# Performance work log

Hardware: AMD Instinct MI355X
Metric: run time of the kernel (lower is better)

The kernel has to match this reference:

```python
import jax, jax.numpy as jnp
import numpy as np


def setup_inputs() -> dict:
    key = jax.random.key(0)
    ks = jax.random.split(key, 5)
    b, c, h, w = 8, 64, 256, 256
    ic = c // 2
    return {
        "x": jax.random.normal(ks[0], (b, c, h, w), dtype=jnp.float32),
        "w_phi": jax.random.normal(ks[1], (ic, c), dtype=jnp.float32) * 0.1,
        "w_theta": jax.random.normal(ks[2], (ic, c), dtype=jnp.float32) * 0.1,
        "w_g": jax.random.normal(ks[3], (ic, c), dtype=jnp.float32) * 0.1,
        "w_mask": jax.random.normal(ks[4], (c, ic), dtype=jnp.float32) * 0.1,
    }


def _conv1x1(x, wgt):
    # bias-free 1x1 conv == channel matmul: (b,c,h,w) x (o,c) -> (b,o,h,w)
    return jnp.einsum('bchw,oc->bohw', x, wgt)


def reference(x, w_phi, w_theta, w_g, w_mask):
    b, c, h, w = x.shape
    ic = c // 2
    n = (h * w) // 2  # per-row length after the quirky view(b, c, -1) of a (b, c/2, h*w) tensor

    # phi and g: conv -> flatten -> global softmax over all c/2*h*w entries -> view (b, c, n)
    phi1 = jax.nn.softmax(_conv1x1(x, w_phi).reshape(b, -1), axis=1).reshape(b, c, n)
    g1 = jax.nn.softmax(_conv1x1(x, w_g).reshape(b, -1), axis=1).reshape(b, c, n)
    theta = _conv1x1(x, w_theta).reshape(b, c, n)

    # y = g1 @ phi1^T @ theta : (b,c,c) then (b,c,n)
    att = jnp.einsum('bcn,bdn->bcd', g1, phi1)
    y = jnp.einsum('bcd,bdn->bcn', att, theta)

    f_s = y.reshape(b, ic, h, w)
    return jnp.einsum('bihw,oi->bohw', f_s, w_mask)
```

## Files before the change

kernel.cpp:

```cpp
#include <hip/hip_runtime.h>

typedef __attribute__((ext_vector_type(8))) short short8;
typedef __attribute__((ext_vector_type(4))) float f32x4;
typedef __attribute__((ext_vector_type(4))) unsigned int uint4v;

#define HW 65536
#define NPOS 32768

__device__ __forceinline__ unsigned short f2bf(float f) {
  unsigned u = __builtin_bit_cast(unsigned, f);
  u += 0x7fffu + ((u >> 16) & 1u);
  return (unsigned short)(u >> 16);
}
__device__ __forceinline__ float bf2f(unsigned short h) {
  unsigned u = (unsigned)h << 16;
  return __builtin_bit_cast(float, u);
}
__device__ __forceinline__ int slot4(int r) { return (r ^ (r >> 2)) & 15; }
__device__ __forceinline__ short8 ld_e16(const unsigned short* p) {
  const uint2 a = *(const uint2*)p;
  const uint2 b = *(const uint2*)(p + 4);
  uint4v u = {a.x, a.y, b.x, b.y};
  return __builtin_bit_cast(short8, u);
}

__global__ __launch_bounds__(256) void k0_prep(
    const float* __restrict__ wphi, const float* __restrict__ wg,
    unsigned short* __restrict__ Whi, unsigned short* __restrict__ Wlo)
{
  const int idx = blockIdx.x * 256 + threadIdx.x;
  const int u = idx >> 6, c = idx & 63;
  const float w = (u < 32) ? wphi[u * 64 + c] : wg[(u - 32) * 64 + c];
  const unsigned short h = f2bf(w);
  Whi[idx] = h;
  Wlo[idx] = f2bf(w - bf2f(h));
}

__global__ __launch_bounds__(256) void k1_att(
    const float* __restrict__ x, const unsigned short* __restrict__ Whi,
    const unsigned short* __restrict__ Wlo, float* __restrict__ attP,
    float2* __restrict__ spart)
{
  __shared__ unsigned short E[2][128 * 68];
  __shared__ float2 rbuf[4];

  const int tid = threadIdx.x;
  const int b = blockIdx.y, blk = blockIdx.x;
  const int w = tid >> 6, l = tid & 63;
  const int lr = l & 15, g = l >> 4;
  const int h = w >> 1, qb = (w & 1) * 2;
  const int n0 = blk * 256;
  const float* xb = x + (size_t)b * 64 * HW + (size_t)h * NPOS;

  short8 wbh[4][2], wbl[4][2];
  #pragma unroll
  for (int cht = 0; cht < 4; ++cht)
    #pragma unroll
    for (int ks = 0; ks < 2; ++ks) {
      const size_t off = (size_t)(cht * 16 + lr) * 64 + ks * 32 + g * 8;
      wbh[cht][ks] = *(const short8*)(Whi + off);
      wbl[cht][ks] = *(const short8*)(Wlo + off);
    }

  f32x4 aacc[4] = {{0.f,0.f,0.f,0.f},{0.f,0.f,0.f,0.f},{0.f,0.f,0.f,0.f},{0.f,0.f,0.f,0.f}};
  float ssp = 0.f, ssg = 0.f;

  float xvA[16], xvB[16];
  #pragma unroll
  for (int e = 0; e < 16; ++e) {
    const size_t co = (size_t)((e >> 3) * 32 + g * 8 + (e & 7)) * HW;
    xvA[e] = xb[co + n0 + (qb + 0) * 16 + lr];
    xvB[e] = xb[co + n0 + (qb + 1) * 16 + lr];
  }

  for (int t = 0; t < 4; ++t) {
    const int buf = t & 1;
    #pragma unroll
    for (int j = 0; j < 2; ++j) {
      const float* xv = j ? xvB : xvA;
      short8 ah[2];
      #pragma unroll
      for (int ks = 0; ks < 2; ++ks)
        #pragma unroll
        for (int e = 0; e < 8; ++e)
          ah[ks][e] = (short)f2bf(xv[ks * 8 + e]);
      f32x4 cacc[4] = {{0.f,0.f,0.f,0.f},{0.f,0.f,0.f,0.f},{0.f,0.f,0.f,0.f},{0.f,0.f,0.f,0.f}};
      #pragma unroll
      for (int cht = 0; cht < 4; ++cht)
        #pragma unroll
        for (int ks = 0; ks < 2; ++ks) {
          cacc[cht] = __builtin_amdgcn_mfma_f32_16x16x32_bf16(ah[ks], wbh[cht][ks], cacc[cht], 0, 0, 0);
          cacc[cht] = __builtin_amdgcn_mfma_f32_16x16x32_bf16(ah[ks], wbl[cht][ks], cacc[cht], 0, 0, 0);
        }
      #pragma unroll
      for (int cht = 0; cht < 4; ++cht) {
        const float e0 = __expf(cacc[cht][0]);
        const float e1 = __expf(cacc[cht][1]);
        const float e2 = __expf(cacc[cht][2]);
        const float e3 = __expf(cacc[cht][3]);
        if (cht < 2) ssp += (e0 + e1) + (e2 + e3);
        else         ssg += (e0 + e1) + (e2 + e3);
        const int row = ((cht >= 2) ? 64 : 0) + 2 * ((cht & 1) * 16 + lr) + h;
        uint2 pk;
        pk.x = (unsigned)f2bf(e0) | ((unsigned)f2bf(e1) << 16);
        pk.y = (unsigned)f2bf(e2) | ((unsigned)f2bf(e3) << 16);
        *(uint2*)&E[buf][row * 68 + (qb + j) * 16 + g * 4] = pk;
      }
    }
    if (t < 3) {
      const int nn = n0 + (t + 1) * 64;
      #pragma unroll
      for (int e = 0; e < 16; ++e) {
        const size_t co = (size_t)((e >> 3) * 32 + g * 8 + (e & 7)) * HW;
        xvA[e] = xb[co + nn + (qb + 0) * 16 + lr];
        xvB[e] = xb[co + nn + (qb + 1) * 16 + lr];
      }
    }
    __syncthreads();

    #pragma unroll
    for (int ks = 0; ks < 2; ++ks) {
      const short8 ag = ld_e16(&E[buf][(64 + w * 16 + lr) * 68 + ks * 32 + g * 8]);
      #pragma unroll
      for (int j = 0; j < 4; ++j) {
        const short8 bp = ld_e16(&E[buf][(j * 16 + lr) * 68 + ks * 32 + g * 8]);
        aacc[j] = __builtin_amdgcn_mfma_f32_16x16x32_bf16(ag, bp, aacc[j], 0, 0, 0);
      }
    }
  }

  float* ap = attP + (size_t)(b * 128 + blk) * 4096;
  #pragma unroll
  for (int j = 0; j < 4; ++j)
    #pragma unroll
    for (int r = 0; r < 4; ++r)
      ap[(w * 16 + g * 4 + r) * 64 + j * 16 + lr] = aacc[j][r];

  #pragma unroll
  for (int off = 32; off > 0; off >>= 1) {
    ssp += __shfl_down(ssp, off);
    ssg += __shfl_down(ssg, off);
  }
  if (l == 0) rbuf[w] = make_float2(ssp, ssg);
  __syncthreads();
  if (tid == 0) {
    float a = 0.f, c = 0.f;
    #pragma unroll
    for (int i = 0; i < 4; ++i) { a += rbuf[i].x; c += rbuf[i].y; }
    spart[b * 128 + blk] = make_float2(a, c);
  }
}

__global__ __launch_bounds__(256) void k3a_reduce(
    const float* __restrict__ attP, float* __restrict__ attQ)
{
  const int b = blockIdx.x >> 5, part = (blockIdx.x >> 2) & 7, es = blockIdx.x & 3;
  const float* p = attP + (size_t)(b * 128 + part * 16) * 4096 + es * 1024;
  float* q = attQ + (size_t)(b * 8 + part) * 4096 + es * 1024;
  for (int e = threadIdx.x; e < 1024; e += 256) {
    float s0 = 0.f, s1 = 0.f, s2 = 0.f, s3 = 0.f;
    #pragma unroll
    for (int k = 0; k < 16; k += 4) {
      s0 += p[(size_t)k * 4096 + e];
      s1 += p[(size_t)(k + 1) * 4096 + e];
      s2 += p[(size_t)(k + 2) * 4096 + e];
      s3 += p[(size_t)(k + 3) * 4096 + e];
    }
    q[e] = (s0 + s1) + (s2 + s3);
  }
}

__global__ __launch_bounds__(1024) void k3b_nmat(
    const float* __restrict__ attQ, const float2* __restrict__ spart,
    const float* __restrict__ wm, const float* __restrict__ wtheta,
    unsigned short* __restrict__ Nhi, unsigned short* __restrict__ Nlo)
{
  __shared__ float att_s[4096];
  __shared__ float Mp[2][64][64];
  __shared__ float wms[64][32];
  __shared__ float wts[32][64];
  __shared__ float sP[128], sG[128];
  const int tid = threadIdx.x;
  const int b = blockIdx.x;

  if (tid < 512) {
    if (tid < 128) {
      const float2 v = spart[b * 128 + tid];
      sP[tid] = v.x; sG[tid] = v.y;
    }
    if (tid < 256) { for (int k = tid; k < 2048; k += 256) wms[k >> 5][k & 31] = wm[k]; }
    else           { for (int k = tid - 256; k < 2048; k += 256) wts[k >> 6][k & 63] = wtheta[k]; }
  }
  for (int e = tid; e < 4096; e += 1024) {
    const float* p = attQ + (size_t)b * 8 * 4096 + e;
    float s = 0.f;
    #pragma unroll
    for (int q = 0; q < 8; ++q) s += p[(size_t)q * 4096];
    att_s[e] = s;
  }
  __syncthreads();
  #pragma unroll
  for (int s = 64; s > 0; s >>= 1) {
    if (tid < s) { sP[tid] += sP[tid + s]; sG[tid] += sG[tid + s]; }
    __syncthreads();
  }
  for (int idx = tid; idx < 8192; idx += 1024) {
    const int h = idx >> 12, o = (idx >> 6) & 63, d = idx & 63;
    float s = 0.f;
    #pragma unroll
    for (int i = 0; i < 32; ++i)
      s = __builtin_fmaf(wms[o][i], att_s[(2 * i + h) * 64 + d], s);
    Mp[h][o][d] = s;
  }
  __syncthreads();
  const float scale = 1.f / (sP[0] * sG[0]);
  for (int idx = tid; idx < 16384; idx += 1024) {
    const int oo = idx >> 7, cc = idx & 127;
    const int h = oo >> 6, o = oo & 63, e = cc >> 6, c = cc & 63;
    float s = 0.f;
    #pragma unroll
    for (int j = 0; j < 32; ++j)
      s = __builtin_fmaf(Mp[h][o][2 * j + e], wts[j][c], s);
    s *= scale;
    const unsigned short hi = f2bf(s);
    Nhi[(size_t)b * 16384 + idx] = hi;
    Nlo[(size_t)b * 16384 + idx] = f2bf(s - bf2f(hi));
  }
}

__global__ __launch_bounds__(512) void k5_out(
    const float* __restrict__ x, const unsigned short* __restrict__ Nhi,
    const unsigned short* __restrict__ Nlo, float* __restrict__ out)
{
  __shared__ unsigned short Xh[64 * 128];
  const int tid = threadIdx.x;
  const int b = blockIdx.y, n0 = blockIdx.x * 64;
  const int w = tid >> 6, l = tid & 63;
  const int lr = l & 15, g = l >> 4;

  short8 bh[4], bl[4];
  #pragma unroll
  for (int ks = 0; ks < 4; ++ks) {
    const size_t off = (size_t)b * 16384 + (size_t)(w * 16 + lr) * 128 + ks * 32 + g * 8;
    bh[ks] = *(const short8*)(Nhi + off);
    bl[ks] = *(const short8*)(Nlo + off);
  }

  {
    const int ccb = w * 16;
    const int c0 = ccb & 63, e0 = ccb >> 6;
    const float* xp = x + (size_t)b * 64 * HW + (size_t)c0 * HW
                    + (size_t)e0 * NPOS + n0 + l;
    float v[16];
    #pragma unroll
    for (int i = 0; i < 16; ++i) v[i] = xp[(size_t)i * HW];
    short8 pa, pb;
    #pragma unroll
    for (int i = 0; i < 8; ++i) {
      pa[i] = (short)f2bf(v[i]);
      pb[i] = (short)f2bf(v[8 + i]);
    }
    const int s8 = slot4(l) << 3;
    *(short8*)&Xh[l * 128 + (ccb ^ s8)] = pa;
    *(short8*)&Xh[l * 128 + ((ccb + 8) ^ s8)] = pb;
  }
  __syncthreads();

  const int oo = w * 16 + lr;
  float* op = out + (size_t)b * 64 * HW + (size_t)(oo & 63) * HW
            + (size_t)(oo >> 6) * NPOS + n0 + g * 4;

  #pragma unroll
  for (int ct4 = 0; ct4 < 4; ++ct4) {
    f32x4 acc = {0.f, 0.f, 0.f, 0.f};
    const int arow = ct4 * 16 + lr;
    const int sw = slot4(arow) << 3;
    #pragma unroll
    for (int ks = 0; ks < 4; ++ks) {
      const short8 av = *(const short8*)&Xh[arow * 128 + ((ks * 32 + g * 8) ^ sw)];
      acc = __builtin_amdgcn_mfma_f32_16x16x32_bf16(av, bh[ks], acc, 0, 0, 0);
      acc = __builtin_amdgcn_mfma_f32_16x16x32_bf16(av, bl[ks], acc, 0, 0, 0);
    }
    *(float4*)(op + ct4 * 16) = *(float4*)&acc;
  }
}

extern "C" void kernel_launch(void* const* d_in, const int* in_sizes, int n_in,
                              void* d_out, int out_size, void* d_ws, size_t ws_size,
                              hipStream_t stream)
{
  const float* x      = (const float*)d_in[0];
  const float* wphi   = (const float*)d_in[1];
  const float* wtheta = (const float*)d_in[2];
  const float* wg     = (const float*)d_in[3];
  const float* wm     = (const float*)d_in[4];
  float* out = (float*)d_out;

  char* ws = (char*)d_ws;
  float* attP         = (float*)ws;
  unsigned short* Whi = (unsigned short*)(ws + 16777216);
  unsigned short* Wlo = (unsigned short*)(ws + 16785408);
  unsigned short* Nhi = (unsigned short*)(ws + 16793600);
  unsigned short* Nlo = (unsigned short*)(ws + 17055744);
  float2* spart       = (float2*)(ws + 17317888);
  float* attQ         = (float*)(ws + 17326080);

  k0_prep<<<dim3(16), 256, 0, stream>>>(wphi, wg, Whi, Wlo);
  k1_att<<<dim3(128, 8), 256, 0, stream>>>(x, Whi, Wlo, attP, spart);
  k3a_reduce<<<dim3(256), 256, 0, stream>>>(attP, attQ);
  k3b_nmat<<<dim3(8), 1024, 0, stream>>>(attQ, spart, wm, wtheta, Nhi, Nlo);
  k5_out<<<dim3(512, 8), 512, 0, stream>>>(x, Nhi, Nlo, out);
}
```

Before: 118.3 us.

## Store partial attention in bf16 and software-pipeline output kernel over four tiles

The per-block partial attention matrices are now written as bf16 instead of fp32, which halves the workspace traffic between the attention and reduce kernels at some cost in accuracy for those partial sums. The output kernel now processes four 64-position tiles per block. It double-buffers the shared-memory staging and prefetches the next tile's x values into registers while the current tile's MFMAs run. It also loads the Nhi/Nlo weight fragments once per 256 positions instead of once per 64, and launches four times fewer blocks.

```diff
diff --git a/kernel.cpp b/kernel.cpp
--- a/kernel.cpp
+++ b/kernel.cpp
@@ -38,7 +38,7 @@
 
 __global__ __launch_bounds__(256) void k1_att(
     const float* __restrict__ x, const unsigned short* __restrict__ Whi,
-    const unsigned short* __restrict__ Wlo, float* __restrict__ attP,
+    const unsigned short* __restrict__ Wlo, unsigned short* __restrict__ attP,
     float2* __restrict__ spart)
 {
   __shared__ unsigned short E[2][128 * 68];
@@ -129,12 +129,12 @@
     }
   }
 
-  float* ap = attP + (size_t)(b * 128 + blk) * 4096;
+  unsigned short* ap = attP + (size_t)(b * 128 + blk) * 4096;
   #pragma unroll
   for (int j = 0; j < 4; ++j)
     #pragma unroll
     for (int r = 0; r < 4; ++r)
-      ap[(w * 16 + g * 4 + r) * 64 + j * 16 + lr] = aacc[j][r];
+      ap[(w * 16 + g * 4 + r) * 64 + j * 16 + lr] = f2bf(aacc[j][r]);
 
   #pragma unroll
   for (int off = 32; off > 0; off >>= 1) {
@@ -152,19 +152,19 @@
 }
 
 __global__ __launch_bounds__(256) void k3a_reduce(
-    const float* __restrict__ attP, float* __restrict__ attQ)
+    const unsigned short* __restrict__ attP, float* __restrict__ attQ)
 {
   const int b = blockIdx.x >> 5, part = (blockIdx.x >> 2) & 7, es = blockIdx.x & 3;
-  const float* p = attP + (size_t)(b * 128 + part * 16) * 4096 + es * 1024;
+  const unsigned short* p = attP + (size_t)(b * 128 + part * 16) * 4096 + es * 1024;
   float* q = attQ + (size_t)(b * 8 + part) * 4096 + es * 1024;
   for (int e = threadIdx.x; e < 1024; e += 256) {
     float s0 = 0.f, s1 = 0.f, s2 = 0.f, s3 = 0.f;
     #pragma unroll
     for (int k = 0; k < 16; k += 4) {
-      s0 += p[(size_t)k * 4096 + e];
-      s1 += p[(size_t)(k + 1) * 4096 + e];
-      s2 += p[(size_t)(k + 2) * 4096 + e];
-      s3 += p[(size_t)(k + 3) * 4096 + e];
+      s0 += bf2f(p[(size_t)k * 4096 + e]);
+      s1 += bf2f(p[(size_t)(k + 1) * 4096 + e]);
+      s2 += bf2f(p[(size_t)(k + 2) * 4096 + e]);
+      s3 += bf2f(p[(size_t)(k + 3) * 4096 + e]);
     }
     q[e] = (s0 + s1) + (s2 + s3);
   }
@@ -232,9 +232,9 @@
     const float* __restrict__ x, const unsigned short* __restrict__ Nhi,
     const unsigned short* __restrict__ Nlo, float* __restrict__ out)
 {
-  __shared__ unsigned short Xh[64 * 128];
+  __shared__ unsigned short Xh[2][64 * 128];
   const int tid = threadIdx.x;
-  const int b = blockIdx.y, n0 = blockIdx.x * 64;
+  const int b = blockIdx.y, n0 = blockIdx.x * 256;
   const int w = tid >> 6, l = tid & 63;
   const int lr = l & 15, g = l >> 4;
 
@@ -246,42 +246,51 @@
     bl[ks] = *(const short8*)(Nlo + off);
   }
 
-  {
-    const int ccb = w * 16;
-    const int c0 = ccb & 63, e0 = ccb >> 6;
-    const float* xp = x + (size_t)b * 64 * HW + (size_t)c0 * HW
-                    + (size_t)e0 * NPOS + n0 + l;
-    float v[16];
-    #pragma unroll
-    for (int i = 0; i < 16; ++i) v[i] = xp[(size_t)i * HW];
-    short8 pa, pb;
-    #pragma unroll
-    for (int i = 0; i < 8; ++i) {
-      pa[i] = (short)f2bf(v[i]);
-      pb[i] = (short)f2bf(v[8 + i]);
-    }
-    const int s8 = slot4(l) << 3;
-    *(short8*)&Xh[l * 128 + (ccb ^ s8)] = pa;
-    *(short8*)&Xh[l * 128 + ((ccb + 8) ^ s8)] = pb;
-  }
-  __syncthreads();
-
+  const int ccb = w * 16;
+  const int c0 = ccb & 63, e0 = ccb >> 6;
+  const float* xp = x + (size_t)b * 64 * HW + (size_t)c0 * HW
+                  + (size_t)e0 * NPOS + n0 + l;
+  const int s8 = slot4(l) << 3;
   const int oo = w * 16 + lr;
-  float* op = out + (size_t)b * 64 * HW + (size_t)(oo & 63) * HW
-            + (size_t)(oo >> 6) * NPOS + n0 + g * 4;
-
-  #pragma unroll
-  for (int ct4 = 0; ct4 < 4; ++ct4) {
-    f32x4 acc = {0.f, 0.f, 0.f, 0.f};
-    const int arow = ct4 * 16 + lr;
-    const int sw = slot4(arow) << 3;
-    #pragma unroll
-    for (int ks = 0; ks < 4; ++ks) {
-      const short8 av = *(const short8*)&Xh[arow * 128 + ((ks * 32 + g * 8) ^ sw)];
-      acc = __builtin_amdgcn_mfma_f32_16x16x32_bf16(av, bh[ks], acc, 0, 0, 0);
-      acc = __builtin_amdgcn_mfma_f32_16x16x32_bf16(av, bl[ks], acc, 0, 0, 0);
-    }
-    *(float4*)(op + ct4 * 16) = *(float4*)&acc;
+  float* op0 = out + (size_t)b * 64 * HW + (size_t)(oo & 63) * HW
+             + (size_t)(oo >> 6) * NPOS + n0 + g * 4;
+
+  float v[16];
+  #pragma unroll
+  for (int i = 0; i < 16; ++i) v[i] = xp[(size_t)i * HW];
+
+  for (int t = 0; t < 4; ++t) {
+    const int buf = t & 1;
+    {
+      short8 pa, pb;
+      #pragma unroll
+      for (int i = 0; i < 8; ++i) {
+        pa[i] = (short)f2bf(v[i]);
+        pb[i] = (short)f2bf(v[8 + i]);
+      }
+      *(short8*)&Xh[buf][l * 128 + (ccb ^ s8)] = pa;
+      *(short8*)&Xh[buf][l * 128 + ((ccb + 8) ^ s8)] = pb;
+    }
+    if (t < 3) {
+      #pragma unroll
+      for (int i = 0; i < 16; ++i) v[i] = xp[(size_t)i * HW + (t + 1) * 64];
+    }
+    __syncthreads();
+
+    float* op = op0 + t * 64;
+    #pragma unroll
+    for (int ct4 = 0; ct4 < 4; ++ct4) {
+      f32x4 acc = {0.f, 0.f, 0.f, 0.f};
+      const int arow = ct4 * 16 + lr;
+      const int sw = slot4(arow) << 3;
+      #pragma unroll
+      for (int ks = 0; ks < 4; ++ks) {
+        const short8 av = *(const short8*)&Xh[buf][arow * 128 + ((ks * 32 + g * 8) ^ sw)];
+        acc = __builtin_amdgcn_mfma_f32_16x16x32_bf16(av, bh[ks], acc, 0, 0, 0);
+        acc = __builtin_amdgcn_mfma_f32_16x16x32_bf16(av, bl[ks], acc, 0, 0, 0);
+      }
+      *(float4*)(op + ct4 * 16) = *(float4*)&acc;
+    }
   }
 }
 
@@ -297,17 +306,17 @@
   float* out = (float*)d_out;
 
   char* ws = (char*)d_ws;
-  float* attP         = (float*)ws;
-  unsigned short* Whi = (unsigned short*)(ws + 16777216);
-  unsigned short* Wlo = (unsigned short*)(ws + 16785408);
-  unsigned short* Nhi = (unsigned short*)(ws + 16793600);
-  unsigned short* Nlo = (unsigned short*)(ws + 17055744);
-  float2* spart       = (float2*)(ws + 17317888);
-  float* attQ         = (float*)(ws + 17326080);
+  unsigned short* attP = (unsigned short*)ws;
+  unsigned short* Whi = (unsigned short*)(ws + 8388608);
+  unsigned short* Wlo = (unsigned short*)(ws + 8396800);
+  unsigned short* Nhi = (unsigned short*)(ws + 8404992);
+  unsigned short* Nlo = (unsigned short*)(ws + 8667136);
+  float2* spart       = (float2*)(ws + 8929280);
+  float* attQ         = (float*)(ws + 8937472);
 
   k0_prep<<<dim3(16), 256, 0, stream>>>(wphi, wg, Whi, Wlo);
   k1_att<<<dim3(128, 8), 256, 0, stream>>>(x, Whi, Wlo, attP, spart);
   k3a_reduce<<<dim3(256), 256, 0, stream>>>(attP, attQ);
   k3b_nmat<<<dim3(8), 1024, 0, stream>>>(attQ, spart, wm, wtheta, Nhi, Nlo);
-  k5_out<<<dim3(512, 8), 512, 0, stream>>>(x, Nhi, Nlo, out);
-}
+  k5_out<<<dim3(128, 8), 512, 0, stream>>>(x, Nhi, Nlo, out);
+}
```

New measurement: 109.5 us. 7.5% less time.
